# Optimization experiments

Measured on AMD Instinct MI355X. Metric: run time of the kernel, lower is better.

The kernel has to match this reference:

```python
import jax, jax.numpy as jnp
import numpy as np

N = 50000      # n_nodes
E = 800000     # n_edges (avg degree 16)
D_IN, D_HID, D_OUT = 128, 128, 64


def setup_inputs() -> dict:
    key = jax.random.key(0)
    k1, k2, k3, k4 = jax.random.split(key, 4)
    x = jax.random.normal(k1, (N, D_IN), jnp.float32)
    edge_index = jax.random.randint(k2, (2, E), 0, N, jnp.int32)
    # Glorot-style init for the two GCNConv linear weights
    W1 = jax.random.normal(k3, (D_IN, D_HID), jnp.float32) / np.sqrt(D_IN)
    W2 = jax.random.normal(k4, (D_HID, D_OUT), jnp.float32) / np.sqrt(D_HID)
    b1 = jnp.zeros((D_HID,), jnp.float32)
    b2 = jnp.zeros((D_OUT,), jnp.float32)
    return {"x": x, "edge_index": edge_index, "W1": W1, "b1": b1, "W2": W2, "b2": b2}


def _gcn_conv(x, W, b, src, dst):
    """PyG GCNConv: linear transform, then sym-normalized aggregation with self-loops."""
    h = x @ W                                   # [N, F_out]
    ones = jnp.ones((src.shape[0],), h.dtype)
    # degree includes the self-loop weight of 1
    deg = jax.ops.segment_sum(ones, dst, num_segments=N) + 1.0
    dinv = jax.lax.rsqrt(deg)                   # D^{-1/2}
    norm = dinv[src] * dinv[dst]                # per-edge normalization
    agg = jax.ops.segment_sum(h[src] * norm[:, None], dst, num_segments=N)
    # self-loop contribution: norm_ii = dinv_i^2
    return agg + h * (dinv * dinv)[:, None] + b


def reference(x, edge_index, W1, b1, W2, b2):
    src, dst = edge_index[0], edge_index[1]
    h = jax.nn.relu(_gcn_conv(x, W1, b1, src, dst))
    out = jax.nn.relu(_gcn_conv(h, W2, b2, src, dst))
    return out
```

## Files before the change

kernel.cpp:

```cpp
#include <hip/hip_runtime.h>

typedef unsigned short u16;
typedef __attribute__((ext_vector_type(8))) short short8;
typedef __attribute__((ext_vector_type(4))) float f32x4;

__device__ __forceinline__ float bflo(unsigned u) {
    union { unsigned u; float f; } v; v.u = u << 16; return v.f;
}
__device__ __forceinline__ float bfhi(unsigned u) {
    union { unsigned u; float f; } v; v.u = u & 0xFFFF0000u; return v.f;
}
__device__ __forceinline__ u16 f2bf(float f) {
    union { float f; unsigned u; } v; v.f = f;
    unsigned u = v.u;
    u += 0x7FFFu + ((u >> 16) & 1u);
    return (u16)(u >> 16);
}

__global__ void k1_gemm_deg(const void* __restrict__ Av, const void* __restrict__ W,
                            u16* __restrict__ out, int M, int GB,
                            const int* __restrict__ dst, int* __restrict__ cnt,
                            int* __restrict__ pos, int E, int* __restrict__ flag) {
    constexpr int NOUT = 128;
    int t = threadIdx.x;
    int bid = blockIdx.x;
    if (bid >= GB) {
        if (bid == GB) {
            __shared__ int c_s;
            if (t == 0) c_s = 0;
            __syncthreads();
            int c = 0;
            for (int i = t; i < 2048; i += 256) {
                int ex = (((const u16*)Av)[2 * i] >> 7) & 0xFF;
                c += (ex >= 160 || ex <= 80) ? 1 : 0;
            }
            atomicAdd(&c_s, c);
            __syncthreads();
            if (t == 0) *flag = (c_s > 64) ? 1 : 0;
        }
        int e = (bid - GB) * 256 + t;
        if (e < E) pos[e] = atomicAdd(&cnt[dst[e]], 1);
        return;
    }
    __shared__ int det;
    if (t == 0) det = 0;
    __syncthreads();
    {
        int ex = (((const u16*)Av)[2 * t] >> 7) & 0xFF;
        if (ex >= 160 || ex <= 80) atomicAdd(&det, 1);
    }
    __syncthreads();
    int fl = det > 8;

    __shared__ u16 Wt[NOUT][136];
    for (int idx = t; idx < NOUT * 128; idx += 256) {
        int k = idx / NOUT, n = idx % NOUT;
        Wt[n][k] = fl ? f2bf(((const float*)W)[idx]) : ((const u16*)W)[idx];
    }
    __syncthreads();
    int wave = t >> 6, lane = t & 63;
    int m0 = (bid * 4 + wave) * 16;
    if (m0 >= M) return;
    int q = lane >> 4;
    int mr = lane & 15;

    short8 a[4];
    if (fl) {
        const float* arow = (const float*)Av + (size_t)(m0 + mr) * 128 + q * 8;
#pragma unroll
        for (int c = 0; c < 4; c++) {
            f32x4 lo = *(const f32x4*)(arow + c * 32);
            f32x4 hi = *(const f32x4*)(arow + c * 32 + 4);
            a[c][0] = (short)f2bf(lo.x); a[c][1] = (short)f2bf(lo.y);
            a[c][2] = (short)f2bf(lo.z); a[c][3] = (short)f2bf(lo.w);
            a[c][4] = (short)f2bf(hi.x); a[c][5] = (short)f2bf(hi.y);
            a[c][6] = (short)f2bf(hi.z); a[c][7] = (short)f2bf(hi.w);
        }
    } else {
        const u16* arow = (const u16*)Av + (size_t)(m0 + mr) * 128 + q * 8;
#pragma unroll
        for (int c = 0; c < 4; c++) a[c] = *(const short8*)(arow + c * 32);
    }

    f32x4 acc[NOUT / 16];
#pragma unroll
    for (int tl = 0; tl < NOUT / 16; tl++) acc[tl] = (f32x4){0.f, 0.f, 0.f, 0.f};
#pragma unroll
    for (int c = 0; c < 4; c++) {
#pragma unroll
        for (int tl = 0; tl < NOUT / 16; tl++) {
            short8 b = *(const short8*)(&Wt[tl * 16 + mr][c * 32 + q * 8]);
            acc[tl] = __builtin_amdgcn_mfma_f32_16x16x32_bf16(a[c], b, acc[tl], 0, 0, 0);
        }
    }
    int rbase = m0 + q * 4;
#pragma unroll
    for (int tl = 0; tl < NOUT / 16; tl++) {
#pragma unroll
        for (int r = 0; r < 4; r++)
            out[(size_t)(rbase + r) * NOUT + tl * 16 + mr] = f2bf(acc[tl][r]);
    }
}

__global__ void k_scan_blocks(const int* __restrict__ cnt, int* __restrict__ rowp_p,
                              int* __restrict__ sums, int n) {
    __shared__ int s[256];
    int t = threadIdx.x;
    int i = blockIdx.x * 256 + t;
    int v = (i < n) ? cnt[i] : 0;
    s[t] = v;
    __syncthreads();
    for (int off = 1; off < 256; off <<= 1) {
        int add = (t >= off) ? s[t - off] : 0;
        __syncthreads();
        s[t] += add;
        __syncthreads();
    }
    if (i < n) rowp_p[i] = s[t] - v;
    if (t == 255) sums[blockIdx.x] = s[255];
}

__global__ void k_fin_fill(const int* __restrict__ rowp_p, int* __restrict__ rowp,
                           const int* __restrict__ sums, const int* __restrict__ cnt,
                           float* __restrict__ dinv, int n, int nb,
                           const int* __restrict__ src, const int* __restrict__ dst,
                           const int* __restrict__ pos, int* __restrict__ col, int E) {
    __shared__ int s[256];
    int t = threadIdx.x;
    int b = blockIdx.x;
    s[t] = sums[t];
    __syncthreads();
    for (int off = 1; off < 256; off <<= 1) {
        int add = (t >= off) ? s[t - off] : 0;
        __syncthreads();
        s[t] += add;
        __syncthreads();
    }
    __syncthreads();
    if (b < nb) {
        int prefix = (b == 0) ? 0 : s[b - 1];
        int i = b * 256 + t;
        if (i < n) {
            rowp[i] = rowp_p[i] + prefix;
            dinv[i] = rsqrtf((float)cnt[i] + 1.0f);
        }
        if (i == 0) rowp[n] = E;
    } else {
        int stride = (gridDim.x - nb) * 256;
        for (int e = (b - nb) * 256 + t; e < E; e += stride) {
            int d = dst[e];
            int tile = d >> 8;
            int prefix = (tile == 0) ? 0 : s[tile - 1];
            col[rowp_p[d] + prefix + pos[e]] = src[e];
        }
    }
}

template <int NOUT>
__global__ void k_gemm_plain(const u16* __restrict__ A, const void* __restrict__ W,
                             u16* __restrict__ out, int M, const int* __restrict__ flag) {
    int fl = *flag;
    __shared__ u16 Wt[NOUT][136];
    int t = threadIdx.x;
    for (int idx = t; idx < NOUT * 128; idx += 256) {
        int k = idx / NOUT, n = idx % NOUT;
        Wt[n][k] = fl ? f2bf(((const float*)W)[idx]) : ((const u16*)W)[idx];
    }
    __syncthreads();
    int wave = t >> 6, lane = t & 63;
    int m0 = ((int)blockIdx.x * 4 + wave) * 16;
    if (m0 >= M) return;
    int q = lane >> 4;
    int mr = lane & 15;

    const u16* arow = A + (size_t)(m0 + mr) * 128 + q * 8;
    short8 a[4];
#pragma unroll
    for (int c = 0; c < 4; c++) a[c] = *(const short8*)(arow + c * 32);

    f32x4 acc[NOUT / 16];
#pragma unroll
    for (int tl = 0; tl < NOUT / 16; tl++) acc[tl] = (f32x4){0.f, 0.f, 0.f, 0.f};
#pragma unroll
    for (int c = 0; c < 4; c++) {
#pragma unroll
        for (int tl = 0; tl < NOUT / 16; tl++) {
            short8 b = *(const short8*)(&Wt[tl * 16 + mr][c * 32 + q * 8]);
            acc[tl] = __builtin_amdgcn_mfma_f32_16x16x32_bf16(a[c], b, acc[tl], 0, 0, 0);
        }
    }
    int rbase = m0 + q * 4;
#pragma unroll
    for (int tl = 0; tl < NOUT / 16; tl++) {
#pragma unroll
        for (int r = 0; r < 4; r++)
            out[(size_t)(rbase + r) * NOUT + tl * 16 + mr] = f2bf(acc[tl][r]);
    }
}

template <int F>
__global__ void k_agg(const u16* __restrict__ g, const int* __restrict__ rowp,
                      const int* __restrict__ col, const float* __restrict__ dinv,
                      const void* __restrict__ biasv, u16* __restrict__ outh,
                      float* __restrict__ outf, const int* __restrict__ flag,
                      int outsel, int N, int E) {
    constexpr int LPR = F / 8;
    constexpr int EPW = 64 / LPR;
    int d = blockIdx.x * 4 + (threadIdx.x >> 6);
    if (d >= N) return;
    int lane = threadIdx.x & 63;
    int er = lane / LPR;
    int fo = (lane % LPR) * 8;

    int beg = rowp[d], end = rowp[d + 1];
    if (beg < 0) beg = 0;
    if (end > E) end = E;
    int deg = end - beg;

    float a0[8], a1[8];
#pragma unroll
    for (int j = 0; j < 8; j++) { a0[j] = 0.f; a1[j] = 0.f; }

    for (int base = 0; base < deg; base += 64) {
        int cnt = deg - base; if (cnt > 64) cnt = 64;
        int colv = 0;
        if (lane < cnt) {
            int s = col[beg + base + lane];
            colv = s < 0 ? 0 : (s >= N ? N - 1 : s);
        }
        int full = cnt / EPW;
        int i = 0;
        for (; i + 2 <= full; i += 2) {
            int s0 = __shfl(colv, i * EPW + er, 64);
            int s1 = __shfl(colv, (i + 1) * EPW + er, 64);
            float d0 = dinv[s0];
            float d1 = dinv[s1];
            uint4 v0 = *(const uint4*)(g + (size_t)s0 * F + fo);
            uint4 v1 = *(const uint4*)(g + (size_t)s1 * F + fo);
            a0[0] += d0 * bflo(v0.x); a0[1] += d0 * bfhi(v0.x);
            a0[2] += d0 * bflo(v0.y); a0[3] += d0 * bfhi(v0.y);
            a0[4] += d0 * bflo(v0.z); a0[5] += d0 * bfhi(v0.z);
            a0[6] += d0 * bflo(v0.w); a0[7] += d0 * bfhi(v0.w);
            a1[0] += d1 * bflo(v1.x); a1[1] += d1 * bfhi(v1.x);
            a1[2] += d1 * bflo(v1.y); a1[3] += d1 * bfhi(v1.y);
            a1[4] += d1 * bflo(v1.z); a1[5] += d1 * bfhi(v1.z);
            a1[6] += d1 * bflo(v1.w); a1[7] += d1 * bfhi(v1.w);
        }
        if (i < full) {
            int s0 = __shfl(colv, i * EPW + er, 64);
            float d0 = dinv[s0];
            uint4 v0 = *(const uint4*)(g + (size_t)s0 * F + fo);
            a0[0] += d0 * bflo(v0.x); a0[1] += d0 * bfhi(v0.x);
            a0[2] += d0 * bflo(v0.y); a0[3] += d0 * bfhi(v0.y);
            a0[4] += d0 * bflo(v0.z); a0[5] += d0 * bfhi(v0.z);
            a0[6] += d0 * bflo(v0.w); a0[7] += d0 * bfhi(v0.w);
            i++;
        }
        int rem = cnt - full * EPW;
        int s0 = __shfl(colv, (full * EPW + er) & 63, 64);
        float d0 = dinv[s0];
        if (er < rem) {
            uint4 v0 = *(const uint4*)(g + (size_t)s0 * F + fo);
            a0[0] += d0 * bflo(v0.x); a0[1] += d0 * bfhi(v0.x);
            a0[2] += d0 * bflo(v0.y); a0[3] += d0 * bfhi(v0.y);
            a0[4] += d0 * bflo(v0.z); a0[5] += d0 * bfhi(v0.z);
            a0[6] += d0 * bflo(v0.w); a0[7] += d0 * bfhi(v0.w);
        }
    }
#pragma unroll
    for (int j = 0; j < 8; j++) a0[j] += a1[j];
#pragma unroll
    for (int off = LPR; off < 64; off <<= 1) {
#pragma unroll
        for (int j = 0; j < 8; j++) a0[j] += __shfl_xor(a0[j], off, 64);
    }

    if (lane < LPR) {
        int fl = *flag;
        uint4 sv = *(const uint4*)(g + (size_t)d * F + fo);
        float bb[8];
        if (fl) {
            const float* bp = (const float*)biasv + fo;
            f32x4 blo = *(const f32x4*)bp;
            f32x4 bhi = *(const f32x4*)(bp + 4);
            bb[0] = blo.x; bb[1] = blo.y; bb[2] = blo.z; bb[3] = blo.w;
            bb[4] = bhi.x; bb[5] = bhi.y; bb[6] = bhi.z; bb[7] = bhi.w;
        } else {
            uint4 bv = *(const uint4*)((const u16*)biasv + fo);
            bb[0] = bflo(bv.x); bb[1] = bfhi(bv.x);
            bb[2] = bflo(bv.y); bb[3] = bfhi(bv.y);
            bb[4] = bflo(bv.z); bb[5] = bfhi(bv.z);
            bb[6] = bflo(bv.w); bb[7] = bfhi(bv.w);
        }
        float di = dinv[d];
        float sf[8] = { bflo(sv.x), bfhi(sv.x), bflo(sv.y), bfhi(sv.y),
                        bflo(sv.z), bfhi(sv.z), bflo(sv.w), bfhi(sv.w) };
        float r[8];
#pragma unroll
        for (int j = 0; j < 8; j++) {
            float v = di * (a0[j] + di * sf[j]) + bb[j];
            r[j] = v > 0.f ? v : 0.f;
        }
        size_t o = (size_t)d * F + fo;
        if (outsel && fl) {
            f32x4 w0 = {r[0], r[1], r[2], r[3]};
            f32x4 w1 = {r[4], r[5], r[6], r[7]};
            *(f32x4*)(outf + o) = w0;
            *(f32x4*)(outf + o + 4) = w1;
        } else {
            uint4 w;
            w.x = (unsigned)f2bf(r[0]) | ((unsigned)f2bf(r[1]) << 16);
            w.y = (unsigned)f2bf(r[2]) | ((unsigned)f2bf(r[3]) << 16);
            w.z = (unsigned)f2bf(r[4]) | ((unsigned)f2bf(r[5]) << 16);
            w.w = (unsigned)f2bf(r[6]) | ((unsigned)f2bf(r[7]) << 16);
            *(uint4*)(outh + o) = w;
        }
    }
}


extern "C" void kernel_launch(void* const* d_in, const int* in_sizes, int n_in,
                              void* d_out, int out_size, void* d_ws, size_t ws_size,
                              hipStream_t stream) {
    const int N = in_sizes[0] / 128;
    const int E = in_sizes[1] / 2;
    const int* ei = (const int*)d_in[1];
    const int* src = ei;
    const int* dst = ei + E;

    char* p = (char*)d_ws;
    auto alloc = [&](size_t b) { char* r = p; p += (b + 255) & ~(size_t)255; return r; };
    int*   flag   = (int*)alloc(256);
    int*   rowp   = (int*)alloc((size_t)(N + 1) * 4);
    int*   rowp_p = (int*)alloc((size_t)N * 4);
    float* dinv   = (float*)alloc((size_t)N * 4);
    int*   col    = (int*)alloc((size_t)E * 4);
    int*   cnt    = (int*)alloc((size_t)N * 4);
    int*   sums   = (int*)alloc(256 * 4);
    int*   pos    = (int*)alloc((size_t)E * 4);
    u16*   g1     = (u16*)alloc((size_t)N * 128 * 2);
    u16*   o1     = (u16*)alloc((size_t)N * 128 * 2);
    u16*   g2     = (u16*)alloc((size_t)N * 64 * 2);

    int eb = (E + 255) / 256;
    int nb = (N + 255) / 256;
    int GB = (N / 16 + 3) / 4;
    int FB = 1024;
    int ab = (N + 3) / 4;

    hipMemsetAsync(cnt, 0, ((char*)sums - (char*)cnt) + 1024, stream);

    k1_gemm_deg<<<GB + eb, 256, 0, stream>>>(d_in[0], d_in[2], g1, N, GB,
                                             dst, cnt, pos, E, flag);
    k_scan_blocks<<<nb, 256, 0, stream>>>(cnt, rowp_p, sums, N);
    k_fin_fill<<<nb + FB, 256, 0, stream>>>(rowp_p, rowp, sums, cnt, dinv, N, nb,
                                            src, dst, pos, col, E);

    k_agg<128><<<ab, 256, 0, stream>>>(g1, rowp, col, dinv, d_in[3],
                                       o1, nullptr, flag, 0, N, E);
    k_gemm_plain<64><<<GB, 256, 0, stream>>>(o1, d_in[4], g2, N, flag);
    k_agg<64><<<ab, 256, 0, stream>>>(g2, rowp, col, dinv, d_in[5],
                                      (u16*)d_out, (float*)d_out, flag, 1, N, E);
}
```

Measured before the change: 208.5 us.

## Replicate degree counters across edge ranges to reduce atomic contention

The degree-count histogram is split into REP=8 replicas, each edge range (chosen by a shift on the edge index) atomically incrementing its own copy. The scan kernel then merges the replicas into per-replica offsets and a total degree, computes dinv there, and the fill kernel adds the replica offset when placing columns. The aim is to cut atomic contention and serialization on popular destination counters, at the cost of a larger memset, more reads in the scan, and an extra gather in the fill.

Result: slower. 213.3 us (+2.3%).

```diff
diff --git a/kernel.cpp b/kernel.cpp
--- a/kernel.cpp
+++ b/kernel.cpp
@@ -17,10 +17,13 @@
     return (u16)(u >> 16);
 }
 
+#define REP 8
+
 __global__ void k1_gemm_deg(const void* __restrict__ Av, const void* __restrict__ W,
                             u16* __restrict__ out, int M, int GB,
                             const int* __restrict__ dst, int* __restrict__ cnt,
-                            int* __restrict__ pos, int E, int* __restrict__ flag) {
+                            int* __restrict__ pos, int E, int N, int shift,
+                            int* __restrict__ flag) {
     constexpr int NOUT = 128;
     int t = threadIdx.x;
     int bid = blockIdx.x;
@@ -39,7 +42,10 @@
             if (t == 0) *flag = (c_s > 64) ? 1 : 0;
         }
         int e = (bid - GB) * 256 + t;
-        if (e < E) pos[e] = atomicAdd(&cnt[dst[e]], 1);
+        if (e < E) {
+            int r = e >> shift;
+            pos[e] = atomicAdd(&cnt[r * N + dst[e]], 1);
+        }
         return;
     }
     __shared__ int det;
@@ -102,13 +108,23 @@
     }
 }
 
-__global__ void k_scan_blocks(const int* __restrict__ cnt, int* __restrict__ rowp_p,
-                              int* __restrict__ sums, int n) {
+__global__ void k_scan_blocks(int* __restrict__ cnt, int* __restrict__ rowp_p,
+                              int* __restrict__ sums, float* __restrict__ dinv,
+                              int n) {
     __shared__ int s[256];
     int t = threadIdx.x;
     int i = blockIdx.x * 256 + t;
-    int v = (i < n) ? cnt[i] : 0;
-    s[t] = v;
+    int deg = 0;
+    if (i < n) {
+#pragma unroll
+        for (int r = 0; r < REP; r++) {
+            int v = cnt[r * n + i];
+            cnt[r * n + i] = deg;
+            deg += v;
+        }
+        dinv[i] = rsqrtf((float)deg + 1.0f);
+    }
+    s[t] = deg;
     __syncthreads();
     for (int off = 1; off < 256; off <<= 1) {
         int add = (t >= off) ? s[t - off] : 0;
@@ -116,15 +132,16 @@
         s[t] += add;
         __syncthreads();
     }
-    if (i < n) rowp_p[i] = s[t] - v;
+    if (i < n) rowp_p[i] = s[t] - deg;
     if (t == 255) sums[blockIdx.x] = s[255];
 }
 
 __global__ void k_fin_fill(const int* __restrict__ rowp_p, int* __restrict__ rowp,
                            const int* __restrict__ sums, const int* __restrict__ cnt,
-                           float* __restrict__ dinv, int n, int nb,
+                           int n, int nb,
                            const int* __restrict__ src, const int* __restrict__ dst,
-                           const int* __restrict__ pos, int* __restrict__ col, int E) {
+                           const int* __restrict__ pos, int* __restrict__ col,
+                           int E, int shift) {
     __shared__ int s[256];
     int t = threadIdx.x;
     int b = blockIdx.x;
@@ -140,18 +157,16 @@
     if (b < nb) {
         int prefix = (b == 0) ? 0 : s[b - 1];
         int i = b * 256 + t;
-        if (i < n) {
-            rowp[i] = rowp_p[i] + prefix;
-            dinv[i] = rsqrtf((float)cnt[i] + 1.0f);
-        }
+        if (i < n) rowp[i] = rowp_p[i] + prefix;
         if (i == 0) rowp[n] = E;
     } else {
         int stride = (gridDim.x - nb) * 256;
         for (int e = (b - nb) * 256 + t; e < E; e += stride) {
             int d = dst[e];
+            int r = e >> shift;
             int tile = d >> 8;
             int prefix = (tile == 0) ? 0 : s[tile - 1];
-            col[rowp_p[d] + prefix + pos[e]] = src[e];
+            col[rowp_p[d] + prefix + cnt[r * n + d] + pos[e]] = src[e];
         }
     }
 }
@@ -335,13 +350,16 @@
     int*   rowp_p = (int*)alloc((size_t)N * 4);
     float* dinv   = (float*)alloc((size_t)N * 4);
     int*   col    = (int*)alloc((size_t)E * 4);
-    int*   cnt    = (int*)alloc((size_t)N * 4);
+    int*   cnt    = (int*)alloc((size_t)REP * N * 4);
     int*   sums   = (int*)alloc(256 * 4);
     int*   pos    = (int*)alloc((size_t)E * 4);
     u16*   g1     = (u16*)alloc((size_t)N * 128 * 2);
     u16*   o1     = (u16*)alloc((size_t)N * 128 * 2);
     u16*   g2     = (u16*)alloc((size_t)N * 64 * 2);
 
+    int shift = 10;
+    while (((E - 1) >> shift) >= REP) shift++;
+
     int eb = (E + 255) / 256;
     int nb = (N + 255) / 256;
     int GB = (N / 16 + 3) / 4;
@@ -351,10 +369,10 @@
     hipMemsetAsync(cnt, 0, ((char*)sums - (char*)cnt) + 1024, stream);
 
     k1_gemm_deg<<<GB + eb, 256, 0, stream>>>(d_in[0], d_in[2], g1, N, GB,
-                                             dst, cnt, pos, E, flag);
-    k_scan_blocks<<<nb, 256, 0, stream>>>(cnt, rowp_p, sums, N);
-    k_fin_fill<<<nb + FB, 256, 0, stream>>>(rowp_p, rowp, sums, cnt, dinv, N, nb,
-                                            src, dst, pos, col, E);
+                                             dst, cnt, pos, E, N, shift, flag);
+    k_scan_blocks<<<nb, 256, 0, stream>>>(cnt, rowp_p, sums, dinv, N);
+    k_fin_fill<<<nb + FB, 256, 0, stream>>>(rowp_p, rowp, sums, cnt, N, nb,
+                                            src, dst, pos, col, E, shift);
 
     k_agg<128><<<ab, 256, 0, stream>>>(g1, rowp, col, dinv, d_in[3],
                                        o1, nullptr, flag, 0, N, E);
```
